# Optimization experiments

Measured on AMD Instinct MI355X. Metric: run time of the kernel, lower is better.

The kernel has to match this reference:

```python
import jax, jax.numpy as jnp
import numpy as np
import math

NUM_HEADS = 16
HEAD_DIM = 64
D_MODEL = NUM_HEADS * HEAD_DIM  # 1024
B, S = 4, 2048

def setup_inputs() -> dict:
    key = jax.random.key(0)
    ks = jax.random.split(key, 8)
    sd = 1.0 / math.sqrt(D_MODEL)
    return {
        "hidden_states": jax.random.normal(ks[0], (B, S, D_MODEL), jnp.float32),
        "attention_mask": jnp.zeros((B, 1, 1, S), jnp.float32),
        "Wq": jax.random.normal(ks[1], (D_MODEL, D_MODEL), jnp.float32) * sd,
        "bq": jnp.zeros((D_MODEL,), jnp.float32),
        "Wk": jax.random.normal(ks[2], (D_MODEL, D_MODEL), jnp.float32) * sd,
        "bk": jnp.zeros((D_MODEL,), jnp.float32),
        "Wv": jax.random.normal(ks[3], (D_MODEL, D_MODEL), jnp.float32) * sd,
        "bv": jnp.zeros((D_MODEL,), jnp.float32),
    }

def _split_heads(x):
    # [B, S, D] -> [B, H, S, hd]
    b, s, _ = x.shape
    return x.reshape(b, s, NUM_HEADS, HEAD_DIM).transpose(0, 2, 1, 3)

def reference(hidden_states, attention_mask, Wq, bq, Wk, bk, Wv, bv):
    # Linear projections (torch nn.Linear: x @ W.T + b)
    q = _split_heads(hidden_states @ Wq.T + bq)
    k = _split_heads(hidden_states @ Wk.T + bk)
    v = _split_heads(hidden_states @ Wv.T + bv)
    scale = 1.0 / math.sqrt(HEAD_DIM)
    # [B, H, Sq, Sk] attention scores, fully materialized as in the original
    scores = jnp.einsum("bhqd,bhkd->bhqk", q, k) * scale + attention_mask
    # relusq replacement for softmax
    probs = jnp.square(jax.nn.relu(scores))
    ctx = jnp.einsum("bhqk,bhkd->bhqd", probs, v)  # [B, H, S, hd]
    b = ctx.shape[0]
    return ctx.transpose(0, 2, 1, 3).reshape(b, -1, D_MODEL)
```

## Files before the change

kernel.cpp:

```cpp
#include <hip/hip_runtime.h>


typedef __bf16 bf16x8 __attribute__((ext_vector_type(8)));
typedef __bf16 bf16x4 __attribute__((ext_vector_type(4)));
typedef short  s16x4  __attribute__((ext_vector_type(4)));
typedef float  f32x4  __attribute__((ext_vector_type(4)));
typedef float  floatx4 __attribute__((ext_vector_type(4)));

#define MFMA16(a, b, c) __builtin_amdgcn_mfma_f32_16x16x32_bf16(a, b, c, 0, 0, 0)
#define MFMA16K16(a, b, c) \
    __builtin_amdgcn_mfma_f32_16x16x16bf16_1k(a, b, c, 0, 0, 0)

#define WAITCNT_VM2() __builtin_amdgcn_s_waitcnt(0x0F72)
#define BARRIER() __builtin_amdgcn_s_barrier()

__device__ __forceinline__ void glds16(const __bf16* g, __bf16* l) {
    __builtin_amdgcn_global_load_lds(
        (const __attribute__((address_space(1))) void*)g,
        (__attribute__((address_space(3))) void*)l, 16, 0, 0);
}

__global__ __launch_bounds__(256) void convert_kernel(
    const float* __restrict__ X, const float* __restrict__ Wq,
    const float* __restrict__ Wk, const float* __restrict__ Wv,
    __bf16* __restrict__ Xb, __bf16* __restrict__ Wqb,
    __bf16* __restrict__ Wkb, __bf16* __restrict__ Wvb)
{
    int blk = blockIdx.x;
    const float* src; __bf16* dst; size_t base;
    if (blk < 4096)      { src = X;  dst = Xb;  base = (size_t)blk * 2048; }
    else if (blk < 4608) { src = Wq; dst = Wqb; base = (size_t)(blk - 4096) * 2048; }
    else if (blk < 5120) { src = Wk; dst = Wkb; base = (size_t)(blk - 4608) * 2048; }
    else                 { src = Wv; dst = Wvb; base = (size_t)(blk - 5120) * 2048; }
    size_t off = base + (size_t)threadIdx.x * 8;
    floatx4 a = *(const floatx4*)(src + off);
    floatx4 c = *(const floatx4*)(src + off + 4);
    bf16x8 o;
    o[0] = (__bf16)a[0]; o[1] = (__bf16)a[1]; o[2] = (__bf16)a[2]; o[3] = (__bf16)a[3];
    o[4] = (__bf16)c[0]; o[5] = (__bf16)c[1]; o[6] = (__bf16)c[2]; o[7] = (__bf16)c[3];
    *(bf16x8*)(dst + off) = o;
}

__global__ __launch_bounds__(256) void qkv_gemm_kernel(
    const __bf16* __restrict__ Xb,
    const __bf16* __restrict__ Wqb, const __bf16* __restrict__ Wkb,
    const __bf16* __restrict__ Wvb,
    const float* __restrict__ bq, const float* __restrict__ bk,
    const float* __restrict__ bv,
    __bf16* __restrict__ qws, __bf16* __restrict__ kws, __bf16* __restrict__ vws)
{
    __shared__ __bf16 As[128 * 64];
    __shared__ __bf16 Bs[128 * 64];

    const int tid  = threadIdx.x;
    const int lane = tid & 63;
    const int wave = tid >> 6;
    const int wm   = (wave >> 1) * 64;
    const int wn   = (wave & 1) * 64;
    const int quad = lane >> 4;
    const int l16  = lane & 15;
    const int m0   = blockIdx.y * 128;

    const int sel = blockIdx.x >> 3;
    const bool vmode = (sel == 2);
    const __bf16* Wb = (sel == 0) ? Wqb : (sel == 1) ? Wkb : Wvb;
    const float* bias = (sel == 0) ? bq : (sel == 1) ? bk : bv;
    __bf16* outp = (sel == 0) ? qws : (sel == 1) ? kws : vws;
    const int n0 = (blockIdx.x & 7) * 128;

    const __bf16* Pa = vmode ? As : Bs;
    const __bf16* Pb = vmode ? Bs : As;
    const int woffA = vmode ? wm : wn;
    const int woffB = vmode ? wn : wm;

    f32x4 acc[4][4] = {};

    for (int k0 = 0; k0 < 1024; k0 += 64) {
        __syncthreads();
        #pragma unroll
        for (int i = 0; i < 4; ++i) {
            int r = wave * 32 + i * 8 + (lane >> 3);
            int c = (lane & 7) ^ (r & 7);
            glds16(Xb + (size_t)(m0 + r) * 1024 + k0 + c * 8,
                   &As[(wave * 32 + i * 8) * 64]);
            glds16(Wb + (size_t)(n0 + r) * 1024 + k0 + c * 8,
                   &Bs[(wave * 32 + i * 8) * 64]);
        }
        __syncthreads();

        #pragma unroll
        for (int kk8 = 0; kk8 < 8; kk8 += 4) {
            bf16x8 af[4], bfr[4];
            #pragma unroll
            for (int a = 0; a < 4; ++a)
                af[a] = *(const bf16x8*)&Pa[(woffA + a * 16 + l16) * 64 +
                                            (((kk8 + quad) ^ (l16 & 7)) * 8)];
            #pragma unroll
            for (int bb = 0; bb < 4; ++bb)
                bfr[bb] = *(const bf16x8*)&Pb[(woffB + bb * 16 + l16) * 64 +
                                              (((kk8 + quad) ^ (l16 & 7)) * 8)];
            #pragma unroll
            for (int a = 0; a < 4; ++a)
                #pragma unroll
                for (int bb = 0; bb < 4; ++bb)
                    acc[a][bb] = MFMA16(af[a], bfr[bb], acc[a][bb]);
        }
    }

    if (!vmode) {
        #pragma unroll
        for (int a = 0; a < 4; ++a) {
            int n = n0 + woffA + a * 16 + quad * 4;
            floatx4 bv4 = *(const floatx4*)&bias[n];
            int h = n >> 6, d0 = n & 63;
            #pragma unroll
            for (int bb = 0; bb < 4; ++bb) {
                int m = m0 + woffB + bb * 16 + l16;
                int bt = m >> 11, s = m & 2047;
                bf16x4 o;
                #pragma unroll
                for (int r = 0; r < 4; ++r)
                    o[r] = (__bf16)(acc[a][bb][r] + bv4[r]);
                *(bf16x4*)&outp[((size_t)(bt * 16 + h) * 2048 + s) * 64 + d0] = o;
            }
        }
    } else {
        #pragma unroll
        for (int a = 0; a < 4; ++a) {
            int m = m0 + woffA + a * 16 + quad * 4;
            int bt = m >> 11, s0 = m & 2047;
            #pragma unroll
            for (int bb = 0; bb < 4; ++bb) {
                int n = n0 + woffB + bb * 16 + l16;
                float bvv = bias[n];
                int h = n >> 6, d = n & 63;
                bf16x4 o;
                #pragma unroll
                for (int r = 0; r < 4; ++r)
                    o[r] = (__bf16)(acc[a][bb][r] + bvv);
                *(bf16x4*)&outp[((size_t)(bt * 16 + h) * 64 + d) * 2048 + s0] = o;
            }
        }
    }
}

__global__ __launch_bounds__(512, 4) void attn_kernel(
    const __bf16* __restrict__ Q, const __bf16* __restrict__ K,
    const __bf16* __restrict__ Vt, const float* __restrict__ mask,
    float* __restrict__ out)
{
    __shared__ __bf16 Ks[2][64 * 64];
    __shared__ __bf16 Vs[2][64 * 64];

    const int tid  = threadIdx.x;
    const int lane = tid & 63;
    const int wave = tid >> 6;
    const int quad = lane >> 4;
    const int l16  = lane & 15;
    const int bh   = blockIdx.y;
    const int b    = bh >> 4;
    const int h    = bh & 15;
    const int q0   = blockIdx.x * 256 + wave * 32;

    const __bf16* Qb = Q  + (size_t)bh * 2048 * 64;
    const __bf16* Kb = K  + (size_t)bh * 2048 * 64;
    const __bf16* Vb = Vt + (size_t)bh * 64 * 2048;
    const float*  mb = mask + b * 2048;

    const int rb = wave * 8;
    const int sr = rb + (lane >> 3);
    const int sc = ((lane & 7) ^ (sr & 7)) * 8;

    bf16x8 aq[2][2];
    #pragma unroll
    for (int qi = 0; qi < 2; ++qi)
        #pragma unroll
        for (int kcd = 0; kcd < 2; ++kcd)
            aq[qi][kcd] = *(const bf16x8*)(Qb +
                (size_t)(q0 + qi * 16 + l16) * 64 + kcd * 32 + quad * 8);

    f32x4 co[2][4] = {};

    glds16(Kb + (size_t)sr * 64 + sc, &Ks[0][rb * 64]);
    glds16(Vb + (size_t)sr * 2048 + sc, &Vs[0][rb * 64]);

    for (int t = 0; t < 32; ++t) {
        const int k0 = t * 64;
        const int kn = (k0 + 64) & 2047;
        const int nb = (t + 1) & 1;
        glds16(Kb + (size_t)(kn + sr) * 64 + sc, &Ks[nb][rb * 64]);
        glds16(Vb + (size_t)sr * 2048 + kn + sc, &Vs[nb][rb * 64]);
        WAITCNT_VM2();
        BARRIER();

        const __bf16* Kt = &Ks[t & 1][0];
        const __bf16* Vtile = &Vs[t & 1][0];

        bf16x4 pf[4][2];
        #pragma unroll
        for (int ki = 0; ki < 4; ++ki) {
            f32x4 st[2] = {};
            #pragma unroll
            for (int kcd = 0; kcd < 2; ++kcd) {
                int key = ki * 16 + l16;
                bf16x8 ak = *(const bf16x8*)&Kt[key * 64 +
                    (((kcd * 4 + quad) ^ (key & 7)) * 8)];
                #pragma unroll
                for (int qi = 0; qi < 2; ++qi)
                    st[qi] = MFMA16(ak, aq[qi][kcd], st[qi]);
            }
            floatx4 mk = *(const floatx4*)&mb[k0 + ki * 16 + quad * 4];
            #pragma unroll
            for (int qi = 0; qi < 2; ++qi) {
                bf16x4 pv;
                #pragma unroll
                for (int r = 0; r < 4; ++r) {
                    float x = st[qi][r] * 0.125f + mk[r];
                    x = fmaxf(x, 0.0f);
                    pv[r] = (__bf16)(x * x);
                }
                pf[ki][qi] = pv;
            }
        }

        #pragma unroll
        for (int ki = 0; ki < 4; ++ki) {
            bf16x4 vb4[4];
            #pragma unroll
            for (int dt = 0; dt < 4; ++dt) {
                int d = dt * 16 + l16;
                int g = ki * 2 + (quad >> 1);
                vb4[dt] = *(const bf16x4*)&Vtile[d * 64 +
                    ((g ^ (d & 7)) * 8) + (quad & 1) * 4];
            }
            #pragma unroll
            for (int qi = 0; qi < 2; ++qi) {
                s16x4 pa = __builtin_bit_cast(s16x4, pf[ki][qi]);
                #pragma unroll
                for (int dt = 0; dt < 4; ++dt)
                    co[qi][dt] = MFMA16K16(pa,
                        __builtin_bit_cast(s16x4, vb4[dt]), co[qi][dt]);
            }
        }
        BARRIER();
    }

    #pragma unroll
    for (int qi = 0; qi < 2; ++qi)
        #pragma unroll
        for (int r = 0; r < 4; ++r) {
            int q = q0 + qi * 16 + quad * 4 + r;
            float* orow = &out[(((size_t)b * 2048 + q) * 16 + h) * 64];
            #pragma unroll
            for (int dt = 0; dt < 4; ++dt)
                orow[dt * 16 + l16] = co[qi][dt][r];
        }
}

extern "C" void kernel_launch(void* const* d_in, const int* in_sizes, int n_in,
                              void* d_out, int out_size, void* d_ws, size_t ws_size,
                              hipStream_t stream) {
    const float* hidden = (const float*)d_in[0];
    const float* mask   = (const float*)d_in[1];
    const float* Wq     = (const float*)d_in[2];
    const float* bq     = (const float*)d_in[3];
    const float* Wk     = (const float*)d_in[4];
    const float* bk     = (const float*)d_in[5];
    const float* Wv     = (const float*)d_in[6];
    const float* bv     = (const float*)d_in[7];
    float* out = (float*)d_out;

    __bf16* qws = (__bf16*)d_ws;
    __bf16* kws = qws + (size_t)64 * 2048 * 64;
    __bf16* vws = kws + (size_t)64 * 2048 * 64;
    __bf16* Xb  = vws + (size_t)64 * 2048 * 64;
    __bf16* Wqb = Xb  + (size_t)8192 * 1024;
    __bf16* Wkb = Wqb + (size_t)1024 * 1024;
    __bf16* Wvb = Wkb + (size_t)1024 * 1024;

    convert_kernel<<<dim3(5632), dim3(256), 0, stream>>>(hidden, Wq, Wk, Wv,
                                                         Xb, Wqb, Wkb, Wvb);
    qkv_gemm_kernel<<<dim3(24, 64), dim3(256), 0, stream>>>(Xb, Wqb, Wkb, Wvb,
                                                            bq, bk, bv,
                                                            qws, kws, vws);
    attn_kernel<<<dim3(8, 64), dim3(512), 0, stream>>>(qws, kws, vws, mask, out);
}
```

Baseline: 272.3 us.

## Triple-buffer QKV GEMM loads, stage mask in LDS, add MFMA priority hints

```diff
diff --git a/kernel.cpp b/kernel.cpp
--- a/kernel.cpp
+++ b/kernel.cpp
@@ -12,7 +12,9 @@
     __builtin_amdgcn_mfma_f32_16x16x16bf16_1k(a, b, c, 0, 0, 0)
 
 #define WAITCNT_VM2() __builtin_amdgcn_s_waitcnt(0x0F72)
+#define WAITCNT_VM4() __builtin_amdgcn_s_waitcnt(0x0F74)
 #define BARRIER() __builtin_amdgcn_s_barrier()
+#define SETPRIO(p) __builtin_amdgcn_s_setprio(p)
 
 __device__ __forceinline__ void glds16(const __bf16* g, __bf16* l) {
     __builtin_amdgcn_global_load_lds(
@@ -49,8 +51,8 @@
     const float* __restrict__ bv,
     __bf16* __restrict__ qws, __bf16* __restrict__ kws, __bf16* __restrict__ vws)
 {
-    __shared__ __bf16 As[128 * 64];
-    __shared__ __bf16 Bs[128 * 64];
+    __shared__ __bf16 As[3][128 * 32];
+    __shared__ __bf16 Bs[3][128 * 32];
 
     const int tid  = threadIdx.x;
     const int lane = tid & 63;
@@ -68,43 +70,57 @@
     __bf16* outp = (sel == 0) ? qws : (sel == 1) ? kws : vws;
     const int n0 = (blockIdx.x & 7) * 128;
 
-    const __bf16* Pa = vmode ? As : Bs;
-    const __bf16* Pb = vmode ? Bs : As;
     const int woffA = vmode ? wm : wn;
     const int woffB = vmode ? wn : wm;
 
+    const int srow = lane >> 2;
+    const int schk = lane & 3;
+    const int rchk = quad ^ ((l16 >> 1) & 3);
+
     f32x4 acc[4][4] = {};
 
-    for (int k0 = 0; k0 < 1024; k0 += 64) {
-        __syncthreads();
-        #pragma unroll
-        for (int i = 0; i < 4; ++i) {
-            int r = wave * 32 + i * 8 + (lane >> 3);
-            int c = (lane & 7) ^ (r & 7);
-            glds16(Xb + (size_t)(m0 + r) * 1024 + k0 + c * 8,
-                   &As[(wave * 32 + i * 8) * 64]);
-            glds16(Wb + (size_t)(n0 + r) * 1024 + k0 + c * 8,
-                   &Bs[(wave * 32 + i * 8) * 64]);
-        }
-        __syncthreads();
-
-        #pragma unroll
-        for (int kk8 = 0; kk8 < 8; kk8 += 4) {
-            bf16x8 af[4], bfr[4];
-            #pragma unroll
-            for (int a = 0; a < 4; ++a)
-                af[a] = *(const bf16x8*)&Pa[(woffA + a * 16 + l16) * 64 +
-                                            (((kk8 + quad) ^ (l16 & 7)) * 8)];
+    #pragma unroll
+    for (int i = 0; i < 2; ++i) {
+        int rb = wave * 32 + i * 16;
+        int r  = rb + srow;
+        int c  = schk ^ ((r >> 1) & 3);
+        glds16(Xb + (size_t)(m0 + r) * 1024 + c * 8, &As[0][rb * 32]);
+        glds16(Wb + (size_t)(n0 + r) * 1024 + c * 8, &Bs[0][rb * 32]);
+    }
+
+    int bc = 0, bn = 1, bx = 2;
+    for (int s = 0; s < 32; ++s) {
+        const int kn = ((s + 1) & 31) * 32;
+        #pragma unroll
+        for (int i = 0; i < 2; ++i) {
+            int rb = wave * 32 + i * 16;
+            int r  = rb + srow;
+            int c  = schk ^ ((r >> 1) & 3);
+            glds16(Xb + (size_t)(m0 + r) * 1024 + kn + c * 8, &As[bn][rb * 32]);
+            glds16(Wb + (size_t)(n0 + r) * 1024 + kn + c * 8, &Bs[bn][rb * 32]);
+        }
+        WAITCNT_VM4();
+        BARRIER();
+
+        const __bf16* Pa_ = vmode ? &As[bc][0] : &Bs[bc][0];
+        const __bf16* Pb_ = vmode ? &Bs[bc][0] : &As[bc][0];
+
+        SETPRIO(1);
+        bf16x8 af[4], bfr[4];
+        #pragma unroll
+        for (int a = 0; a < 4; ++a)
+            af[a] = *(const bf16x8*)&Pa_[(woffA + a * 16 + l16) * 32 + rchk * 8];
+        #pragma unroll
+        for (int bb = 0; bb < 4; ++bb)
+            bfr[bb] = *(const bf16x8*)&Pb_[(woffB + bb * 16 + l16) * 32 + rchk * 8];
+        #pragma unroll
+        for (int a = 0; a < 4; ++a)
             #pragma unroll
             for (int bb = 0; bb < 4; ++bb)
-                bfr[bb] = *(const bf16x8*)&Pb[(woffB + bb * 16 + l16) * 64 +
-                                              (((kk8 + quad) ^ (l16 & 7)) * 8)];
-            #pragma unroll
-            for (int a = 0; a < 4; ++a)
-                #pragma unroll
-                for (int bb = 0; bb < 4; ++bb)
-                    acc[a][bb] = MFMA16(af[a], bfr[bb], acc[a][bb]);
-        }
+                acc[a][bb] = MFMA16(af[a], bfr[bb], acc[a][bb]);
+        SETPRIO(0);
+
+        int tmp = bc; bc = bn; bn = bx; bx = tmp;
     }
 
     if (!vmode) {
@@ -116,12 +132,12 @@
             #pragma unroll
             for (int bb = 0; bb < 4; ++bb) {
                 int m = m0 + woffB + bb * 16 + l16;
-                int bt = m >> 11, s = m & 2047;
+                int bt = m >> 11, ss = m & 2047;
                 bf16x4 o;
                 #pragma unroll
                 for (int r = 0; r < 4; ++r)
                     o[r] = (__bf16)(acc[a][bb][r] + bv4[r]);
-                *(bf16x4*)&outp[((size_t)(bt * 16 + h) * 2048 + s) * 64 + d0] = o;
+                *(bf16x4*)&outp[((size_t)(bt * 16 + h) * 2048 + ss) * 64 + d0] = o;
             }
         }
     } else {
@@ -151,6 +167,7 @@
 {
     __shared__ __bf16 Ks[2][64 * 64];
     __shared__ __bf16 Vs[2][64 * 64];
+    __shared__ float  Ms[2048];
 
     const int tid  = threadIdx.x;
     const int lane = tid & 63;
@@ -183,10 +200,12 @@
 
     glds16(Kb + (size_t)sr * 64 + sc, &Ks[0][rb * 64]);
     glds16(Vb + (size_t)sr * 2048 + sc, &Vs[0][rb * 64]);
+    glds16((const __bf16*)mb + (size_t)wave * 512 + lane * 8,
+           (__bf16*)Ms + wave * 512);
 
     for (int t = 0; t < 32; ++t) {
         const int k0 = t * 64;
-        const int kn = (k0 + 64) & 2047;
+        const int kn = ((t + 1) & 31) * 64;
         const int nb = (t + 1) & 1;
         glds16(Kb + (size_t)(kn + sr) * 64 + sc, &Ks[nb][rb * 64]);
         glds16(Vb + (size_t)sr * 2048 + kn + sc, &Vs[nb][rb * 64]);
@@ -196,10 +215,10 @@
         const __bf16* Kt = &Ks[t & 1][0];
         const __bf16* Vtile = &Vs[t & 1][0];
 
-        bf16x4 pf[4][2];
+        f32x4 st[4][2] = {};
+        SETPRIO(1);
         #pragma unroll
         for (int ki = 0; ki < 4; ++ki) {
-            f32x4 st[2] = {};
             #pragma unroll
             for (int kcd = 0; kcd < 2; ++kcd) {
                 int key = ki * 16 + l16;
@@ -207,15 +226,21 @@
                     (((kcd * 4 + quad) ^ (key & 7)) * 8)];
                 #pragma unroll
                 for (int qi = 0; qi < 2; ++qi)
-                    st[qi] = MFMA16(ak, aq[qi][kcd], st[qi]);
-            }
-            floatx4 mk = *(const floatx4*)&mb[k0 + ki * 16 + quad * 4];
+                    st[ki][qi] = MFMA16(ak, aq[qi][kcd], st[ki][qi]);
+            }
+        }
+        SETPRIO(0);
+
+        bf16x4 pf[4][2];
+        #pragma unroll
+        for (int ki = 0; ki < 4; ++ki) {
+            floatx4 mk = *(const floatx4*)&Ms[k0 + ki * 16 + quad * 4];
             #pragma unroll
             for (int qi = 0; qi < 2; ++qi) {
                 bf16x4 pv;
                 #pragma unroll
                 for (int r = 0; r < 4; ++r) {
-                    float x = st[qi][r] * 0.125f + mk[r];
+                    float x = st[ki][qi][r] * 0.125f + mk[r];
                     x = fmaxf(x, 0.0f);
                     pv[r] = (__bf16)(x * x);
                 }
@@ -223,6 +248,7 @@
             }
         }
 
+        SETPRIO(1);
         #pragma unroll
         for (int ki = 0; ki < 4; ++ki) {
             bf16x4 vb4[4];
@@ -242,6 +268,7 @@
                         __builtin_bit_cast(s16x4, vb4[dt]), co[qi][dt]);
             }
         }
+        SETPRIO(0);
         BARRIER();
     }
 
```

Result: no change. 268.9 us (-1.3%).
